# Optimization experiments

Measured on AMD Instinct MI355X. Metric: run time of the kernel, lower is better.

The kernel has to match this reference:

```python
import jax, jax.numpy as jnp
import numpy as np

NUM_GRAPHS = 128
NODES_PER_GRAPH = 512
LATENT_DIM = 256


def setup_inputs() -> dict:
    key = jax.random.key(0)
    n_total = NUM_GRAPHS * NODES_PER_GRAPH
    z = jax.random.normal(key, (n_total, LATENT_DIM), dtype=jnp.float32)
    # sorted graph assignment: nodes of graph i are contiguous
    batch = (jnp.arange(n_total, dtype=jnp.int32) // NODES_PER_GRAPH).astype(jnp.int32)
    return {"z": z, "batch": batch, "num_graphs": NUM_GRAPHS, "max_nodes": NODES_PER_GRAPH}


def reference(z, batch, num_graphs, max_nodes):
    # Eval-mode forward (dropout is identity when not training).
    n_total, d = z.shape
    ones = jnp.ones((n_total,), dtype=jnp.int32)
    counts = jax.ops.segment_sum(ones, batch, num_segments=num_graphs)  # [G]
    starts = jnp.concatenate([jnp.zeros((1,), jnp.int32), jnp.cumsum(counts)[:-1].astype(jnp.int32)])
    pos = jnp.arange(n_total, dtype=jnp.int32) - starts[batch]  # intra-graph node index
    # Scatter nodes into zero-padded [G, max_nodes, D] tensor
    z_pad = jnp.zeros((num_graphs, max_nodes, d), dtype=z.dtype).at[batch, pos].set(z)
    valid = jnp.zeros((num_graphs, max_nodes), dtype=bool).at[batch, pos].set(True)
    # Per-graph inner-product decoder + sigmoid, padded positions forced to 0
    adj = jax.nn.sigmoid(jnp.einsum('gnd,gmd->gnm', z_pad, z_pad))  # [G, N, N]
    mask = valid[:, :, None] & valid[:, None, :]
    return jnp.where(mask, adj, jnp.zeros((), dtype=adj.dtype))
```

## Files before the change

### kernel.cpp

```cpp
#include <hip/hip_runtime.h>

typedef __fp16 fp16x2 __attribute__((ext_vector_type(2)));
typedef _Float16 half8 __attribute__((ext_vector_type(8)));
typedef float floatx4 __attribute__((ext_vector_type(4)));

namespace {

constexpr int NODES = 512;
constexpr int DIM   = 256;
constexpr int BM    = 128;
constexpr int BK    = 64;

union Cvt8 { fp16x2 h2[4]; half8 h8; };

__device__ inline half8 pack8(const floatx4 f0, const floatx4 f1) {
  Cvt8 c;
  c.h2[0] = __builtin_amdgcn_cvt_pkrtz(f0.x, f0.y);
  c.h2[1] = __builtin_amdgcn_cvt_pkrtz(f0.z, f0.w);
  c.h2[2] = __builtin_amdgcn_cvt_pkrtz(f1.x, f1.y);
  c.h2[3] = __builtin_amdgcn_cvt_pkrtz(f1.z, f1.w);
  return c.h8;
}

__device__ inline half8 pack8(const float4 f0, const float4 f1) {
  Cvt8 c;
  c.h2[0] = __builtin_amdgcn_cvt_pkrtz(f0.x, f0.y);
  c.h2[1] = __builtin_amdgcn_cvt_pkrtz(f0.z, f0.w);
  c.h2[2] = __builtin_amdgcn_cvt_pkrtz(f1.x, f1.y);
  c.h2[3] = __builtin_amdgcn_cvt_pkrtz(f1.z, f1.w);
  return c.h8;
}

__device__ inline void async_ld16(const void* g, void* lds) {
  __builtin_amdgcn_global_load_lds(
      (const __attribute__((address_space(1))) unsigned int*)g,
      (__attribute__((address_space(3))) unsigned int*)lds,
      16, 0, 0);
}

__global__ __launch_bounds__(256)
void cvt_kernel(const float* __restrict__ z, _Float16* __restrict__ z16) {
  const int b = blockIdx.x;
  const int x = b & 7;
  const int j = b >> 3;
  const int g = x + 8 * (j >> 6);
  const int chunk = j & 63;
  const size_t base = ((size_t)g * NODES + (size_t)chunk * 8) * DIM
                    + (size_t)threadIdx.x * 8;
  const floatx4* p = reinterpret_cast<const floatx4*>(z + base);
  const floatx4 f0 = __builtin_nontemporal_load(p);
  const floatx4 f1 = __builtin_nontemporal_load(p + 1);
  *reinterpret_cast<half8*>(z16 + base) = pack8(f0, f1);
}

__global__ __launch_bounds__(256, 4)
void gemm_kernel(const _Float16* __restrict__ z16, float* __restrict__ out) {
  __shared__ __align__(16) _Float16 As[BM * BK];
  __shared__ __align__(16) _Float16 Bs[BM * BK];

  const int bid = blockIdx.x;
  const int g    = (bid & 7) + 8 * (bid >> 7);
  const int tile = (bid >> 3) & 15;
  const int tn   = tile >> 2;
  const int tm   = tile & 3;

  const int tid  = threadIdx.x;
  const int lane = tid & 63;
  const int wave = tid >> 6;
  const int wRow = wave >> 1;
  const int wCol = wave & 1;
  const int lrow = lane & 15;
  const int quad = lane >> 4;

  const _Float16* zA = z16 + ((size_t)g * NODES + tn * BM) * DIM;
  const _Float16* zB = z16 + ((size_t)g * NODES + tm * BM) * DIM;

  const int sRow = lane >> 3;
  const int sCp  = (lane & 7) ^ sRow;
  const size_t sOffH = (size_t)sRow * DIM + sCp * 8;

  floatx4 acc[4][4];
#pragma unroll
  for (int i = 0; i < 4; ++i)
#pragma unroll
    for (int j = 0; j < 4; ++j)
      acc[i][j] = (floatx4){0.f, 0.f, 0.f, 0.f};

  for (int kk = 0; kk < DIM; kk += BK) {
#pragma unroll
    for (int it = 0; it < 4; ++it) {
      const int q = wave * 4 + it;
      const _Float16* gA = zA + (size_t)q * 8 * DIM + kk + sOffH;
      const _Float16* gB = zB + (size_t)q * 8 * DIM + kk + sOffH;
      async_ld16(gA, &As[q * 512]);
      async_ld16(gB, &Bs[q * 512]);
    }
    __syncthreads();

#pragma unroll
    for (int ks = 0; ks < 2; ++ks) {
      half8 af[4], bf[4];
#pragma unroll
      for (int i = 0; i < 4; ++i) {
        const int row = wRow * 64 + i * 16 + lrow;
        const int cp = (ks * 4 + quad) ^ (lrow & 7);
        af[i] = *reinterpret_cast<const half8*>(&As[row * BK + cp * 8]);
      }
#pragma unroll
      for (int j = 0; j < 4; ++j) {
        const int row = wCol * 64 + j * 16 + lrow;
        const int cp = (ks * 4 + quad) ^ (lrow & 7);
        bf[j] = *reinterpret_cast<const half8*>(&Bs[row * BK + cp * 8]);
      }
#pragma unroll
      for (int i = 0; i < 4; ++i)
#pragma unroll
        for (int j = 0; j < 4; ++j)
          acc[i][j] = __builtin_amdgcn_mfma_f32_16x16x32_f16(af[i], bf[j], acc[i][j], 0, 0, 0);
    }
    __syncthreads();
  }

  float* outg = out + (size_t)g * NODES * NODES;
  const int nBase = tn * BM + wRow * 64;
  const int mBase = tm * BM + wCol * 64;
#pragma unroll
  for (int j = 0; j < 4; ++j) {
    const int m = mBase + j * 16 + lrow;
    float* rowp = outg + (size_t)m * NODES;
#pragma unroll
    for (int i = 0; i < 4; ++i) {
      const int n0 = nBase + i * 16 + quad * 4;
      floatx4 v;
#pragma unroll
      for (int r = 0; r < 4; ++r) {
        const float x = acc[i][j][r];
        v[r] = __builtin_amdgcn_rcpf(1.0f + __expf(-x));
      }
      __builtin_nontemporal_store(v, reinterpret_cast<floatx4*>(rowp + n0));
    }
  }
}

constexpr int LSTR = 72;
__global__ __launch_bounds__(256, 4)
void fallback_kernel(const float* __restrict__ z, float* __restrict__ out) {
  __shared__ _Float16 As[BM * LSTR];
  __shared__ _Float16 Bs[BM * LSTR];
  const int bid = blockIdx.x;
  const int g    = (bid & 7) + 8 * (bid >> 7);
  const int tile = (bid >> 3) & 15;
  const int tn   = tile >> 2;
  const int tm   = tile & 3;
  const int tid  = threadIdx.x;
  const int lane = tid & 63;
  const int wave = tid >> 6;
  const int wRow = wave >> 1;
  const int wCol = wave & 1;
  const int lrow = lane & 15;
  const int quad = lane >> 4;
  const float* zA = z + ((size_t)g * NODES + tn * BM) * DIM;
  const float* zB = z + ((size_t)g * NODES + tm * BM) * DIM;
  const int srow  = tid >> 1;
  const int shalf = tid & 1;
  floatx4 acc[4][4];
#pragma unroll
  for (int i = 0; i < 4; ++i)
#pragma unroll
    for (int j = 0; j < 4; ++j)
      acc[i][j] = (floatx4){0.f, 0.f, 0.f, 0.f};
  for (int kk = 0; kk < DIM; kk += BK) {
    {
      const float4* pa = reinterpret_cast<const float4*>(zA + srow * DIM + kk + shalf * 32);
      _Float16* da = &As[srow * LSTR + shalf * 32];
      float4 f0 = pa[0], f1 = pa[1], f2 = pa[2], f3 = pa[3];
      *reinterpret_cast<half8*>(da)     = pack8(f0, f1);
      *reinterpret_cast<half8*>(da + 8) = pack8(f2, f3);
      f0 = pa[4]; f1 = pa[5]; f2 = pa[6]; f3 = pa[7];
      *reinterpret_cast<half8*>(da + 16) = pack8(f0, f1);
      *reinterpret_cast<half8*>(da + 24) = pack8(f2, f3);
    }
    {
      const float4* pb = reinterpret_cast<const float4*>(zB + srow * DIM + kk + shalf * 32);
      _Float16* db = &Bs[srow * LSTR + shalf * 32];
      float4 f0 = pb[0], f1 = pb[1], f2 = pb[2], f3 = pb[3];
      *reinterpret_cast<half8*>(db)     = pack8(f0, f1);
      *reinterpret_cast<half8*>(db + 8) = pack8(f2, f3);
      f0 = pb[4]; f1 = pb[5]; f2 = pb[6]; f3 = pb[7];
      *reinterpret_cast<half8*>(db + 16) = pack8(f0, f1);
      *reinterpret_cast<half8*>(db + 24) = pack8(f2, f3);
    }
    __syncthreads();
#pragma unroll
    for (int ks = 0; ks < 2; ++ks) {
      half8 af[4], bf[4];
#pragma unroll
      for (int i = 0; i < 4; ++i)
        af[i] = *reinterpret_cast<const half8*>(
            &As[(wRow * 64 + i * 16 + lrow) * LSTR + ks * 32 + quad * 8]);
#pragma unroll
      for (int j = 0; j < 4; ++j)
        bf[j] = *reinterpret_cast<const half8*>(
            &Bs[(wCol * 64 + j * 16 + lrow) * LSTR + ks * 32 + quad * 8]);
#pragma unroll
      for (int i = 0; i < 4; ++i)
#pragma unroll
        for (int j = 0; j < 4; ++j)
          acc[i][j] = __builtin_amdgcn_mfma_f32_16x16x32_f16(af[i], bf[j], acc[i][j], 0, 0, 0);
    }
    __syncthreads();
  }
  float* outg = out + (size_t)g * NODES * NODES;
  const int nBase = tn * BM + wRow * 64;
  const int mBase = tm * BM + wCol * 64;
#pragma unroll
  for (int j = 0; j < 4; ++j) {
    const int m = mBase + j * 16 + lrow;
    float* rowp = outg + (size_t)m * NODES;
#pragma unroll
    for (int i = 0; i < 4; ++i) {
      const int n0 = nBase + i * 16 + quad * 4;
      floatx4 v;
#pragma unroll
      for (int r = 0; r < 4; ++r) {
        const float x = acc[i][j][r];
        v[r] = __builtin_amdgcn_rcpf(1.0f + __expf(-x));
      }
      __builtin_nontemporal_store(v, reinterpret_cast<floatx4*>(rowp + n0));
    }
  }
}

}

extern "C" void kernel_launch(void* const* d_in, const int* in_sizes, int n_in,
                              void* d_out, int out_size, void* d_ws, size_t ws_size,
                              hipStream_t stream) {
  const float* z = (const float*)d_in[0];
  float* out = (float*)d_out;
  const size_t need = (size_t)128 * 512 * 256 * sizeof(_Float16);
  if (ws_size >= need) {
    _Float16* z16 = (_Float16*)d_ws;
    hipLaunchKernelGGL(cvt_kernel, dim3(8192), dim3(256), 0, stream, z, z16);
    hipLaunchKernelGGL(gemm_kernel, dim3(128 * 16), dim3(256), 0, stream, z16, out);
  } else {
    hipLaunchKernelGGL(fallback_kernel, dim3(128 * 16), dim3(256), 0, stream, z, out);
  }
}
```

Baseline: 232.2 us.

## Exploit Gram matrix symmetry: compute upper-triangle tiles and mirror stores

Launches only the 10 upper-triangular 128x128 tiles per graph instead of 16 and writes each off-diagonal tile's sigmoid result both normally and transposed. Diagonal tiles load only one operand into LDS and reuse it for both sides. This cuts MFMA work and input loads by about 40%. In exchange, the transposed writes are scalar, strided stores, and the nontemporal hint is dropped on the main stores.

```diff
diff --git a/kernel.cpp b/kernel.cpp
--- a/kernel.cpp
+++ b/kernel.cpp
@@ -36,6 +36,10 @@
       (const __attribute__((address_space(1))) unsigned int*)g,
       (__attribute__((address_space(3))) unsigned int*)lds,
       16, 0, 0);
+}
+
+__device__ inline float sigmoidf(float x) {
+  return __builtin_amdgcn_rcpf(1.0f + __expf(-x));
 }
 
 __global__ __launch_bounds__(256)
@@ -59,10 +63,18 @@
   __shared__ __align__(16) _Float16 Bs[BM * BK];
 
   const int bid = blockIdx.x;
-  const int g    = (bid & 7) + 8 * (bid >> 7);
-  const int tile = (bid >> 3) & 15;
-  const int tn   = tile >> 2;
-  const int tm   = tile & 3;
+  const int x    = bid & 7;
+  const int j    = bid >> 3;
+  const int ggrp = j / 10;
+  const int t    = j - ggrp * 10;
+  const int g    = x + 8 * ggrp;
+
+  int tn, tm;
+  if (t < 4)      { tn = 0; tm = t; }
+  else if (t < 7) { tn = 1; tm = t - 3; }
+  else if (t < 9) { tn = 2; tm = t - 5; }
+  else            { tn = 3; tm = 3; }
+  const bool diag = (tn == tm);
 
   const int tid  = threadIdx.x;
   const int lane = tid & 63;
@@ -79,21 +91,25 @@
   const int sCp  = (lane & 7) ^ sRow;
   const size_t sOffH = (size_t)sRow * DIM + sCp * 8;
 
+  const _Float16* Bsrc = diag ? As : Bs;
+
   floatx4 acc[4][4];
 #pragma unroll
   for (int i = 0; i < 4; ++i)
 #pragma unroll
-    for (int j = 0; j < 4; ++j)
-      acc[i][j] = (floatx4){0.f, 0.f, 0.f, 0.f};
+    for (int jj = 0; jj < 4; ++jj)
+      acc[i][jj] = (floatx4){0.f, 0.f, 0.f, 0.f};
 
   for (int kk = 0; kk < DIM; kk += BK) {
 #pragma unroll
     for (int it = 0; it < 4; ++it) {
       const int q = wave * 4 + it;
       const _Float16* gA = zA + (size_t)q * 8 * DIM + kk + sOffH;
-      const _Float16* gB = zB + (size_t)q * 8 * DIM + kk + sOffH;
       async_ld16(gA, &As[q * 512]);
-      async_ld16(gB, &Bs[q * 512]);
+      if (!diag) {
+        const _Float16* gB = zB + (size_t)q * 8 * DIM + kk + sOffH;
+        async_ld16(gB, &Bs[q * 512]);
+      }
     }
     __syncthreads();
 
@@ -107,16 +123,16 @@
         af[i] = *reinterpret_cast<const half8*>(&As[row * BK + cp * 8]);
       }
 #pragma unroll
-      for (int j = 0; j < 4; ++j) {
-        const int row = wCol * 64 + j * 16 + lrow;
+      for (int jj = 0; jj < 4; ++jj) {
+        const int row = wCol * 64 + jj * 16 + lrow;
         const int cp = (ks * 4 + quad) ^ (lrow & 7);
-        bf[j] = *reinterpret_cast<const half8*>(&Bs[row * BK + cp * 8]);
+        bf[jj] = *reinterpret_cast<const half8*>(&Bsrc[row * BK + cp * 8]);
       }
 #pragma unroll
       for (int i = 0; i < 4; ++i)
 #pragma unroll
-        for (int j = 0; j < 4; ++j)
-          acc[i][j] = __builtin_amdgcn_mfma_f32_16x16x32_f16(af[i], bf[j], acc[i][j], 0, 0, 0);
+        for (int jj = 0; jj < 4; ++jj)
+          acc[i][jj] = __builtin_amdgcn_mfma_f32_16x16x32_f16(af[i], bf[jj], acc[i][jj], 0, 0, 0);
     }
     __syncthreads();
   }
@@ -125,19 +141,22 @@
   const int nBase = tn * BM + wRow * 64;
   const int mBase = tm * BM + wCol * 64;
 #pragma unroll
-  for (int j = 0; j < 4; ++j) {
-    const int m = mBase + j * 16 + lrow;
+  for (int jj = 0; jj < 4; ++jj) {
+    const int m = mBase + jj * 16 + lrow;
     float* rowp = outg + (size_t)m * NODES;
 #pragma unroll
     for (int i = 0; i < 4; ++i) {
       const int n0 = nBase + i * 16 + quad * 4;
       floatx4 v;
 #pragma unroll
-      for (int r = 0; r < 4; ++r) {
-        const float x = acc[i][j][r];
-        v[r] = __builtin_amdgcn_rcpf(1.0f + __expf(-x));
-      }
-      __builtin_nontemporal_store(v, reinterpret_cast<floatx4*>(rowp + n0));
+      for (int r = 0; r < 4; ++r)
+        v[r] = sigmoidf(acc[i][jj][r]);
+      *reinterpret_cast<floatx4*>(rowp + n0) = v;
+      if (!diag) {
+#pragma unroll
+        for (int r = 0; r < 4; ++r)
+          outg[(size_t)(n0 + r) * NODES + m] = v[r];
+      }
     }
   }
 }
@@ -214,19 +233,16 @@
   const int nBase = tn * BM + wRow * 64;
   const int mBase = tm * BM + wCol * 64;
 #pragma unroll
-  for (int j = 0; j < 4; ++j) {
-    const int m = mBase + j * 16 + lrow;
-    float* rowp = outg + (size_t)m * NODES;
-#pragma unroll
-    for (int i = 0; i < 4; ++i) {
-      const int n0 = nBase + i * 16 + quad * 4;
-      floatx4 v;
+  for (int i = 0; i < 4; ++i) {
+#pragma unroll
+    for (int j = 0; j < 4; ++j) {
+      const int m = mBase + j * 16 + lrow;
 #pragma unroll
       for (int r = 0; r < 4; ++r) {
+        const int n = nBase + i * 16 + quad * 4 + r;
         const float x = acc[i][j][r];
-        v[r] = __builtin_amdgcn_rcpf(1.0f + __expf(-x));
-      }
-      __builtin_nontemporal_store(v, reinterpret_cast<floatx4*>(rowp + n0));
+        outg[(size_t)n * NODES + m] = sigmoidf(x);
+      }
     }
   }
 }
@@ -242,7 +258,7 @@
   if (ws_size >= need) {
     _Float16* z16 = (_Float16*)d_ws;
     hipLaunchKernelGGL(cvt_kernel, dim3(8192), dim3(256), 0, stream, z, z16);
-    hipLaunchKernelGGL(gemm_kernel, dim3(128 * 16), dim3(256), 0, stream, z16, out);
+    hipLaunchKernelGGL(gemm_kernel, dim3(128 * 10), dim3(256), 0, stream, z16, out);
   } else {
     hipLaunchKernelGGL(fallback_kernel, dim3(128 * 16), dim3(256), 0, stream, z, out);
   }
```

Result: no change. 229.7 us (-1.1%).
